# Kernel tuning notes

Hardware: AMD Instinct MI355X
Metric: run time of the kernel (lower is better)

## Reference

```python
import jax, jax.numpy as jnp
import numpy as np

E, TOPK = 8, 2
B, S, D, H = 2, 4096, 1024, 2048


def setup_inputs() -> dict:
    key = jax.random.key(0)
    k1, k2, k3, k4, k5 = jax.random.split(key, 5)
    x = jax.random.normal(k1, (B, S, D), dtype=jnp.float32)
    expert_p = jax.random.uniform(k2, (B * S, TOPK), dtype=jnp.float32)
    expert_idxs = jax.random.randint(k3, (B * S, TOPK), 0, E)
    # experts.weight = stack(cat([w1, w3], dim=1)) -> [E, D, 2H]
    w13 = jax.random.normal(k4, (E, D, 2 * H), dtype=jnp.float32) * 0.02
    # output_experts.weight = stack(w2) -> [E, H, D]
    w2 = jax.random.normal(k5, (E, H, D), dtype=jnp.float32) * 0.02
    return {"x": x, "expert_p": expert_p, "expert_idxs": expert_idxs, "w13": w13, "w2": w2}


def reference(x, expert_p, expert_idxs, w13, w2):
    # Faithful math of FusedExperts.forward:
    #   per routed pair (t, k) with expert e = expert_idxs[t, k]:
    #     hg = x_t @ w13[e];  h, g = split(hg)   (h from w1, g from w3)
    #     y_t += expert_p[t, k] * (silu(g) * h) @ w2[e]
    # Expressed as a small static loop over experts with per-token routing mask
    # (the original's sort/grouped-GEMM/scatter is a kernel-level optimization
    # of exactly this computation).
    x_shape = x.shape
    xf = x.reshape(-1, x_shape[-1])  # [T, D]
    n_experts = w13.shape[0]
    y = jnp.zeros_like(xf)
    for e in range(n_experts):
        hg = xf @ w13[e]                       # [T, 2H]
        h, g = jnp.split(hg, 2, axis=-1)       # w1 out, w3 out
        he = jax.nn.silu(g) * h                # [T, H]
        ye = he @ w2[e]                        # [T, D]
        pe = jnp.sum(expert_p * (expert_idxs == e), axis=-1)  # [T]
        y = y + pe[:, None] * ye
    return y.reshape(x_shape)
```

## Files before the change

### kernel.cpp

```cpp
#include <hip/hip_runtime.h>
#include <cstdint>
#include <cstddef>

#define TT   8192
#define DD   1024
#define HH   2048
#define H2   4096
#define EE   8
#define PP   16384
#define PADROWS 17280
#define MAXTILES 135

typedef unsigned short u16;
typedef __attribute__((ext_vector_type(8))) short bf16x8;
typedef __attribute__((ext_vector_type(8))) unsigned short u16x8;
typedef __attribute__((ext_vector_type(4))) float f32x4;

__device__ __forceinline__ u16 f2bf(float f) {
  unsigned int u = __builtin_bit_cast(unsigned int, f);
  u += 0x7fffu + ((u >> 16) & 1u);
  return (u16)(u >> 16);
}
__device__ __forceinline__ float bf2f(u16 s) {
  unsigned int u = ((unsigned int)s) << 16;
  return __builtin_bit_cast(float, u);
}

__device__ __forceinline__ void gload_lds16(const u16* g, u16* l) {
  __builtin_amdgcn_global_load_lds(
      (const __attribute__((address_space(1))) void*)g,
      (__attribute__((address_space(3))) void*)l, 16, 0, 0);
}

__global__ __launch_bounds__(256)
void prep_kernel(const float* __restrict__ x, u16* __restrict__ xb,
                 const float* __restrict__ w13, u16* __restrict__ w13t,
                 const float* __restrict__ w2, u16* __restrict__ w2t,
                 const int* __restrict__ eidx, const float* __restrict__ ep,
                 int* __restrict__ pofs, int* __restrict__ ptok,
                 float* __restrict__ pscale, int* __restrict__ ppos) {
  __shared__ __align__(16) u16 tile[32][140];
  __shared__ int hcnt[EE], hbase[EE], hrun[EE];
  const int b = blockIdx.x;
  const int t = threadIdx.x;

  if (b < 4096) {
    const long i = (long)b * 256 + t;
    const f32x4* s = (const f32x4*)(x + i * 8);
    f32x4 a = s[0], c = s[1];
    u16x8 o;
    o[0]=f2bf(a[0]); o[1]=f2bf(a[1]); o[2]=f2bf(a[2]); o[3]=f2bf(a[3]);
    o[4]=f2bf(c[0]); o[5]=f2bf(c[1]); o[6]=f2bf(c[2]); o[7]=f2bf(c[3]);
    *(u16x8*)(xb + i * 8) = o;
    return;
  }

  if (b < 16384) {
    const float* src; u16* dst; int R, C, gx, gy, gz;
    if (b < 12288) {
      const int lb = b - 4096;
      src = w13; dst = w13t; R = DD; C = H2;
      gx = lb & 127; gy = (lb >> 7) & 7; gz = lb >> 10;
    } else {
      const int lb = b - 12288;
      src = w2; dst = w2t; R = HH; C = DD;
      gx = lb & 31; gy = (lb >> 5) & 15; gz = lb >> 9;
    }
    const long base = (long)gz * (long)R * C;
    const int c0 = gx * 32, r0 = gy * 128;
    {
      const int tx = t & 31, ty = t >> 5;
#pragma unroll
      for (int rr = 0; rr < 16; ++rr) {
        const int r = ty + rr * 8;
        tile[tx][r] = f2bf(src[base + (long)(r0 + r) * C + c0 + tx]);
      }
    }
    __syncthreads();
    {
      const int k = t & 15, cb = t >> 4;
#pragma unroll
      for (int i = 0; i < 2; ++i) {
        const int c = i * 16 + cb;
        u16x8 o = *(const u16x8*)(&tile[c][8 * k]);
        *(u16x8*)(dst + base + (long)(c0 + c) * R + r0 + 8 * k) = o;
      }
    }
    return;
  }

  if (t < EE) { hcnt[t] = 0; hrun[t] = 0; }
  __syncthreads();
#pragma unroll 4
  for (int k = 0; k < 64; ++k) {
    const int i = t * 64 + k;
    atomicAdd(&hcnt[eidx[i]], 1);
  }
  __syncthreads();
  if (t == 0) {
    int run = 0;
#pragma unroll
    for (int e = 0; e < EE; ++e) {
      pofs[e] = run; hbase[e] = run;
      run += ((hcnt[e] + 127) >> 7) << 7;
    }
    pofs[EE] = run;
  }
  __syncthreads();
#pragma unroll 4
  for (int k = 0; k < 64; ++k) {
    const int i = t * 64 + k;
    const int e = eidx[i];
    const int r = atomicAdd(&hrun[e], 1);
    const int pos = hbase[e] + r;
    ptok[pos] = i >> 1;
    pscale[pos] = ep[i];
    ppos[i] = pos;
  }
}

__global__ __launch_bounds__(256, 2)
void gemm1_kernel(const u16* __restrict__ xb, const u16* __restrict__ w13t,
                  const int* __restrict__ ptok, const int* __restrict__ pofs,
                  u16* __restrict__ hb) {
  __shared__ __align__(16) u16 lds_a[128 * 64];
  __shared__ __align__(16) u16 lds_b[128 * 64];

  const int f = blockIdx.y * MAXTILES + blockIdx.x;
  const int wg = (f & 7) * 540 + (f >> 3);
  const int tileIdx = wg % MAXTILES;
  const int j = wg / MAXTILES;

  const int ts = tileIdx * 128;
  if (ts >= pofs[EE]) return;
  int e = 0;
#pragma unroll
  for (int i = 1; i < EE; ++i) e += (ts >= pofs[i]) ? 1 : 0;

  const int tid = threadIdx.x;
  const int w = tid >> 6, lane = tid & 63;
  const int wr = w >> 1, wc = w & 1;

  const u16* bbase = w13t + (long)e * ((long)H2 * DD);

  const u16* asrc[4]; const u16* bsrc[4];
  u16* adst[4]; u16* bdst[4];
#pragma unroll
  for (int r = 0; r < 4; ++r) {
    const int L = (r * 4 + w) * 1024 + lane * 16;
    const int row = L >> 7;
    const int slot = ((L >> 4) & 7) ^ (row & 7);
    asrc[r] = xb + (long)ptok[ts + row] * DD + slot * 8;
    const int gr = (row < 64) ? (j * 64 + row) : (HH + j * 64 + row - 64);
    bsrc[r] = bbase + (long)gr * DD + slot * 8;
    adst[r] = lds_a + (r * 4 + w) * 512;
    bdst[r] = lds_b + (r * 4 + w) * 512;
  }

  const int rA = wr * 64 + (lane & 15);
  const int sA = lane >> 4;
  const int x7 = lane & 7;
  int aoff[2][4], boff[2][4];
  int rB[4];
  rB[0] = wc * 32 + (lane & 15);
  rB[1] = wc * 32 + 16 + (lane & 15);
  rB[2] = 64 + wc * 32 + (lane & 15);
  rB[3] = 64 + wc * 32 + 16 + (lane & 15);
#pragma unroll
  for (int kk = 0; kk < 2; ++kk) {
    const int sl = ((kk * 4 + sA) ^ x7) * 8;
#pragma unroll
    for (int m = 0; m < 4; ++m) aoff[kk][m] = (rA + m * 16) * 64 + sl;
#pragma unroll
    for (int n = 0; n < 4; ++n) boff[kk][n] = rB[n] * 64 + sl;
  }

  f32x4 acc[4][4];
#pragma unroll
  for (int m = 0; m < 4; ++m)
#pragma unroll
    for (int n = 0; n < 4; ++n) acc[m][n] = (f32x4){0.f, 0.f, 0.f, 0.f};

  for (int k0 = 0; k0 < DD; k0 += 64) {
#pragma unroll
    for (int r = 0; r < 4; ++r) gload_lds16(asrc[r] + k0, adst[r]);
#pragma unroll
    for (int r = 0; r < 4; ++r) gload_lds16(bsrc[r] + k0, bdst[r]);
    __syncthreads();

    bf16x8 af[2][4], bfr[2][4];
#pragma unroll
    for (int kk = 0; kk < 2; ++kk) {
#pragma unroll
      for (int m = 0; m < 4; ++m) af[kk][m] = *(const bf16x8*)(lds_a + aoff[kk][m]);
#pragma unroll
      for (int n = 0; n < 4; ++n) bfr[kk][n] = *(const bf16x8*)(lds_b + boff[kk][n]);
    }
#pragma unroll
    for (int m = 0; m < 4; ++m)
#pragma unroll
      for (int n = 0; n < 4; ++n)
#pragma unroll
        for (int kk = 0; kk < 2; ++kk)
          acc[m][n] = __builtin_amdgcn_mfma_f32_16x16x32_bf16(af[kk][m], bfr[kk][n], acc[m][n], 0, 0, 0);
    __syncthreads();
  }

  const int rg = lane >> 4;
#pragma unroll
  for (int m = 0; m < 4; ++m)
#pragma unroll
    for (int n = 0; n < 2; ++n) {
      const int col = j * 64 + wc * 32 + n * 16 + (lane & 15);
#pragma unroll
      for (int r = 0; r < 4; ++r) {
        const int row = ts + wr * 64 + m * 16 + rg * 4 + r;
        const float h = acc[m][n][r];
        const float g = acc[m][n + 2][r];
        hb[(long)row * HH + col] = f2bf(h * (g / (1.f + __expf(-g))));
      }
    }
}

__global__ __launch_bounds__(256, 2)
void gemm2_kernel(const u16* __restrict__ hb, const u16* __restrict__ w2t,
                  const float* __restrict__ pscale, const int* __restrict__ pofs,
                  u16* __restrict__ ye) {
  __shared__ __align__(16) u16 lds_a[128 * 64];
  __shared__ __align__(16) u16 lds_b[256 * 64];

  const int f = blockIdx.y * 136 + blockIdx.x;
  const int k8 = f & 7, idx = f >> 3;
  const int tileIdx = (k8 & 1) * 68 + idx;
  const int j = k8 >> 1;

  const int ts = tileIdx * 128;
  if (ts >= pofs[EE]) return;
  int e = 0;
#pragma unroll
  for (int i = 1; i < EE; ++i) e += (ts >= pofs[i]) ? 1 : 0;

  const int tid = threadIdx.x;
  const int w = tid >> 6, lane = tid & 63;
  const int wr = w >> 1, wc = w & 1;

  const u16* bbase = w2t + (long)e * ((long)DD * HH);

  const u16* asrc[4]; const u16* bsrc[8];
  u16* adst[4]; u16* bdst[8];
#pragma unroll
  for (int r = 0; r < 4; ++r) {
    const int L = r * 4096 + tid * 16;
    const int row = L >> 7;
    const int slot = ((L >> 4) & 7) ^ (row & 7);
    asrc[r] = hb + (long)(ts + row) * HH + slot * 8;
    adst[r] = lds_a + r * 2048 + w * 512;
  }
#pragma unroll
  for (int r = 0; r < 8; ++r) {
    const int L = r * 4096 + tid * 16;
    const int row = L >> 7;
    const int slot = ((L >> 4) & 7) ^ (row & 7);
    bsrc[r] = bbase + (long)(j * 256 + row) * HH + slot * 8;
    bdst[r] = lds_b + r * 2048 + w * 512;
  }

  const int l15 = lane & 15, x7 = lane & 7, sA = lane >> 4;
  int aoff[2][4], boff[2][8];
#pragma unroll
  for (int kk = 0; kk < 2; ++kk) {
    const int sl = ((kk * 4 + sA) ^ x7) * 8;
#pragma unroll
    for (int m = 0; m < 4; ++m) aoff[kk][m] = (wr * 64 + m * 16 + l15) * 64 + sl;
#pragma unroll
    for (int n = 0; n < 8; ++n) boff[kk][n] = (wc * 128 + n * 16 + l15) * 64 + sl;
  }

  f32x4 acc[4][8];
#pragma unroll
  for (int m = 0; m < 4; ++m)
#pragma unroll
    for (int n = 0; n < 8; ++n) acc[m][n] = (f32x4){0.f, 0.f, 0.f, 0.f};

  for (int k0 = 0; k0 < HH; k0 += 64) {
#pragma unroll
    for (int r = 0; r < 4; ++r) gload_lds16(asrc[r] + k0, adst[r]);
#pragma unroll
    for (int r = 0; r < 8; ++r) gload_lds16(bsrc[r] + k0, bdst[r]);
    __syncthreads();

    bf16x8 af[2][4], bfr[2][8];
#pragma unroll
    for (int kk = 0; kk < 2; ++kk) {
#pragma unroll
      for (int m = 0; m < 4; ++m) af[kk][m] = *(const bf16x8*)(lds_a + aoff[kk][m]);
#pragma unroll
      for (int n = 0; n < 8; ++n) bfr[kk][n] = *(const bf16x8*)(lds_b + boff[kk][n]);
    }
#pragma unroll
    for (int m = 0; m < 4; ++m)
#pragma unroll
      for (int n = 0; n < 8; ++n)
#pragma unroll
        for (int kk = 0; kk < 2; ++kk)
          acc[m][n] = __builtin_amdgcn_mfma_f32_16x16x32_bf16(af[kk][m], bfr[kk][n], acc[m][n], 0, 0, 0);
    __syncthreads();
  }

#pragma unroll
  for (int m = 0; m < 4; ++m)
#pragma unroll
    for (int r = 0; r < 4; ++r) {
      const int row = ts + wr * 64 + m * 16 + sA * 4 + r;
      const float sc = pscale[row];
#pragma unroll
      for (int n = 0; n < 8; ++n) {
        const int col = j * 256 + wc * 128 + n * 16 + l15;
        ye[(long)row * DD + col] = f2bf(acc[m][n][r] * sc);
      }
    }
}

__global__ void combine_kernel(const u16* __restrict__ ye, const int* __restrict__ ppos,
                               float* __restrict__ y) {
  const long i = (long)blockIdx.x * 256 + threadIdx.x;
  const int t = (int)(i >> 7);
  const int c = ((int)i & 127) * 8;
  const int p0 = ppos[t * 2], p1 = ppos[t * 2 + 1];
  u16x8 v0 = *(const u16x8*)(ye + (long)p0 * DD + c);
  u16x8 v1 = *(const u16x8*)(ye + (long)p1 * DD + c);
  f32x4 o0, o1;
  o0[0] = bf2f(v0[0]) + bf2f(v1[0]);
  o0[1] = bf2f(v0[1]) + bf2f(v1[1]);
  o0[2] = bf2f(v0[2]) + bf2f(v1[2]);
  o0[3] = bf2f(v0[3]) + bf2f(v1[3]);
  o1[0] = bf2f(v0[4]) + bf2f(v1[4]);
  o1[1] = bf2f(v0[5]) + bf2f(v1[5]);
  o1[2] = bf2f(v0[6]) + bf2f(v1[6]);
  o1[3] = bf2f(v0[7]) + bf2f(v1[7]);
  *(f32x4*)(y + (long)t * DD + c) = o0;
  *(f32x4*)(y + (long)t * DD + c + 4) = o1;
}

extern "C" void kernel_launch(void* const* d_in, const int* in_sizes, int n_in,
                              void* d_out, int out_size, void* d_ws, size_t ws_size,
                              hipStream_t stream) {
  const float* x    = (const float*)d_in[0];
  const float* ep   = (const float*)d_in[1];
  const int*   eidx = (const int*)d_in[2];
  const float* w13  = (const float*)d_in[3];
  const float* w2   = (const float*)d_in[4];
  float* y = (float*)d_out;

  char* ws = (char*)d_ws;
  size_t off = 0;
  auto alloc = [&](size_t bytes) {
    char* p = ws + off;
    off = (off + bytes + 255) & ~(size_t)255;
    return p;
  };
  u16* xb     = (u16*)alloc((size_t)TT * DD * 2);
  u16* w13t   = (u16*)alloc((size_t)EE * H2 * DD * 2);
  u16* w2t    = (u16*)alloc((size_t)EE * DD * HH * 2);
  u16* hb     = (u16*)alloc((size_t)PADROWS * HH * 2);
  u16* ye     = (u16*)alloc((size_t)PADROWS * DD * 2);
  char* zbase = ws + off;
  int*   ptok   = (int*)alloc((size_t)PADROWS * 4);
  float* pscale = (float*)alloc((size_t)PADROWS * 4);
  size_t zbytes = (size_t)((ws + off) - zbase);
  int*   pofs   = (int*)alloc((EE + 1) * 4);
  int*   ppos   = (int*)alloc((size_t)PP * 4);
  (void)ws_size; (void)in_sizes; (void)n_in; (void)out_size;

  hipMemsetAsync(zbase, 0, zbytes, stream);

  prep_kernel<<<16385, 256, 0, stream>>>(x, xb, w13, w13t, w2, w2t,
                                         eidx, ep, pofs, ptok, pscale, ppos);

  gemm1_kernel<<<dim3(MAXTILES, HH / 64), 256, 0, stream>>>(xb, w13t, ptok, pofs, hb);
  gemm2_kernel<<<dim3(136, 4), 256, 0, stream>>>(hb, w2t, pscale, pofs, ye);
  combine_kernel<<<4096, 256, 0, stream>>>(ye, ppos, y);
}
```

Measured before the change: 358.1 us.

## Rewrite gemm1 as 256x256 tile, 8-wave, double-buffered pipelined MFMA kernel

gemm1 now uses 512 threads and a 256-row by 128-column (h/g interleaved) tile with a 128 KB double-buffered LDS ring. Global-to-LDS loads for the next K-steps are interleaved between quarter blocks of MFMAs, using explicit vmcnt/lgkmcnt waits, barriers and setprio. The goal is to hide load latency and raise arithmetic intensity per tile. Expert groups are padded to 256 rows to match, and gemm2's grid remap is adjusted for the new padding. This adds padding waste and relies on delicate manual synchronization, with only one block able to fit per CU.

```diff
diff --git a/kernel.cpp b/kernel.cpp
--- a/kernel.cpp
+++ b/kernel.cpp
@@ -8,8 +8,8 @@
 #define H2   4096
 #define EE   8
 #define PP   16384
-#define PADROWS 17280
-#define MAXTILES 135
+#define PADROWS 18432
+#define MAXT1 72
 
 typedef unsigned short u16;
 typedef __attribute__((ext_vector_type(8))) short bf16x8;
@@ -31,6 +31,11 @@
       (const __attribute__((address_space(1))) void*)g,
       (__attribute__((address_space(3))) void*)l, 16, 0, 0);
 }
+
+#define BAR()    __builtin_amdgcn_s_barrier()
+#define LGKM0()  asm volatile("s_waitcnt lgkmcnt(0)")
+#define WAITV4() asm volatile("s_waitcnt vmcnt(4)" ::: "memory")
+#define WAITV0() asm volatile("s_waitcnt vmcnt(0)" ::: "memory")
 
 __global__ __launch_bounds__(256)
 void prep_kernel(const float* __restrict__ x, u16* __restrict__ xb,
@@ -102,7 +107,7 @@
 #pragma unroll
     for (int e = 0; e < EE; ++e) {
       pofs[e] = run; hbase[e] = run;
-      run += ((hcnt[e] + 127) >> 7) << 7;
+      run += ((hcnt[e] + 255) >> 8) << 8;
     }
     pofs[EE] = run;
   }
@@ -119,19 +124,28 @@
   }
 }
 
-__global__ __launch_bounds__(256, 2)
+#define QUAD(M0, N0) do {                                                        \
+    __builtin_amdgcn_s_setprio(1);                                               \
+    _Pragma("unroll") for (int mm = 0; mm < 4; ++mm)                             \
+    _Pragma("unroll") for (int nn = 0; nn < 2; ++nn)                             \
+    _Pragma("unroll") for (int kk = 0; kk < 2; ++kk)                             \
+      acc[(M0)+mm][(N0)+nn] = __builtin_amdgcn_mfma_f32_16x16x32_bf16(           \
+          af[kk][(M0)+mm], bf[kk][(N0)+nn], acc[(M0)+mm][(N0)+nn], 0, 0, 0);     \
+    __builtin_amdgcn_s_setprio(0);                                               \
+  } while (0)
+
+__global__ __launch_bounds__(512)
 void gemm1_kernel(const u16* __restrict__ xb, const u16* __restrict__ w13t,
                   const int* __restrict__ ptok, const int* __restrict__ pofs,
                   u16* __restrict__ hb) {
-  __shared__ __align__(16) u16 lds_a[128 * 64];
-  __shared__ __align__(16) u16 lds_b[128 * 64];
-
-  const int f = blockIdx.y * MAXTILES + blockIdx.x;
-  const int wg = (f & 7) * 540 + (f >> 3);
-  const int tileIdx = wg % MAXTILES;
-  const int j = wg / MAXTILES;
-
-  const int ts = tileIdx * 128;
+  __shared__ __align__(16) u16 lds[65536];
+
+  const int f = blockIdx.y * MAXT1 + blockIdx.x;
+  const int wg = (f & 7) * 144 + (f >> 3);
+  const int tileIdx = wg % MAXT1;
+  const int j = wg / MAXT1;
+
+  const int ts = tileIdx * 256;
   if (ts >= pofs[EE]) return;
   int e = 0;
 #pragma unroll
@@ -139,82 +153,109 @@
 
   const int tid = threadIdx.x;
   const int w = tid >> 6, lane = tid & 63;
-  const int wr = w >> 1, wc = w & 1;
+  const int wm = w >> 2, wn = w & 3;
 
   const u16* bbase = w13t + (long)e * ((long)H2 * DD);
 
-  const u16* asrc[4]; const u16* bsrc[4];
-  u16* adst[4]; u16* bdst[4];
-#pragma unroll
-  for (int r = 0; r < 4; ++r) {
-    const int L = (r * 4 + w) * 1024 + lane * 16;
-    const int row = L >> 7;
-    const int slot = ((L >> 4) & 7) ^ (row & 7);
-    asrc[r] = xb + (long)ptok[ts + row] * DD + slot * 8;
-    const int gr = (row < 64) ? (j * 64 + row) : (HH + j * 64 + row - 64);
-    bsrc[r] = bbase + (long)gr * DD + slot * 8;
-    adst[r] = lds_a + (r * 4 + w) * 512;
-    bdst[r] = lds_b + (r * 4 + w) * 512;
-  }
-
-  const int rA = wr * 64 + (lane & 15);
-  const int sA = lane >> 4;
-  const int x7 = lane & 7;
-  int aoff[2][4], boff[2][4];
-  int rB[4];
-  rB[0] = wc * 32 + (lane & 15);
-  rB[1] = wc * 32 + 16 + (lane & 15);
-  rB[2] = 64 + wc * 32 + (lane & 15);
-  rB[3] = 64 + wc * 32 + 16 + (lane & 15);
+  int aoffg[2][2]; int boffg[2][2]; int dstA[2][2], dstB[2][2];
+#pragma unroll
+  for (int ht = 0; ht < 2; ++ht)
+#pragma unroll
+    for (int i = 0; i < 2; ++i) {
+      const int L = tid * 16 + i * 8192;
+      const int row = L >> 7;
+      const int slot = ((L >> 4) & 7) ^ (row & 7);
+      aoffg[ht][i] = ptok[ts + ht * 128 + row] * DD + slot * 8;
+      const int r = ht * 128 + row;
+      const int wnr = r >> 6, within = r & 63;
+      const int grow = (within < 32) ? (j * 128 + wnr * 32 + within)
+                                     : (HH + j * 128 + wnr * 32 + within - 32);
+      boffg[ht][i] = grow * DD + slot * 8;
+      dstA[ht][i] = ht * 8192 + i * 4096 + w * 512;
+      dstB[ht][i] = 32768 + ht * 8192 + i * 4096 + w * 512;
+    }
+
+  const int l15 = lane & 15, x7 = lane & 7, sA = lane >> 4;
+  int aoff[2][8], boff[2][4];
 #pragma unroll
   for (int kk = 0; kk < 2; ++kk) {
     const int sl = ((kk * 4 + sA) ^ x7) * 8;
 #pragma unroll
-    for (int m = 0; m < 4; ++m) aoff[kk][m] = (rA + m * 16) * 64 + sl;
-#pragma unroll
-    for (int n = 0; n < 4; ++n) boff[kk][n] = rB[n] * 64 + sl;
-  }
-
-  f32x4 acc[4][4];
-#pragma unroll
-  for (int m = 0; m < 4; ++m)
+    for (int m = 0; m < 8; ++m) aoff[kk][m] = (m * 16 + l15) * 64 + sl;
+#pragma unroll
+    for (int n = 0; n < 4; ++n) boff[kk][n] = ((w & 1) * 64 + n * 16 + l15) * 64 + sl;
+  }
+
+  f32x4 acc[8][4];
+#pragma unroll
+  for (int m = 0; m < 8; ++m)
 #pragma unroll
     for (int n = 0; n < 4; ++n) acc[m][n] = (f32x4){0.f, 0.f, 0.f, 0.f};
 
-  for (int k0 = 0; k0 < DD; k0 += 64) {
-#pragma unroll
-    for (int r = 0; r < 4; ++r) gload_lds16(asrc[r] + k0, adst[r]);
-#pragma unroll
-    for (int r = 0; r < 4; ++r) gload_lds16(bsrc[r] + k0, bdst[r]);
-    __syncthreads();
-
-    bf16x8 af[2][4], bfr[2][4];
+  auto stageA = [&](int t, int p, int ht) {
+    const int k0 = t * 64;
+    gload_lds16(xb + aoffg[ht][0] + k0, lds + p * 16384 + dstA[ht][0]);
+    gload_lds16(xb + aoffg[ht][1] + k0, lds + p * 16384 + dstA[ht][1]);
+  };
+  auto stageB = [&](int t, int p, int ht) {
+    const int k0 = t * 64;
+    gload_lds16(bbase + boffg[ht][0] + k0, lds + p * 16384 + dstB[ht][0]);
+    gload_lds16(bbase + boffg[ht][1] + k0, lds + p * 16384 + dstB[ht][1]);
+  };
+
+  bf16x8 af[2][8], bf[2][4];
+
+  stageA(0, 0, 0); stageA(0, 0, 1); stageB(0, 0, 0); stageB(0, 0, 1);
+  stageA(1, 1, 0); stageA(1, 1, 1);
+  WAITV4(); BAR();
+
+  for (int t = 0; t < 16; ++t) {
+    const int p = t & 1;
+    const bool stB = t < 15, stA = t < 14;
+    const u16* Areg = lds + p * 16384 + wm * 8192;
+    const u16* Breg = lds + 32768 + p * 16384 + (wn >> 1) * 8192;
 #pragma unroll
     for (int kk = 0; kk < 2; ++kk) {
 #pragma unroll
-      for (int m = 0; m < 4; ++m) af[kk][m] = *(const bf16x8*)(lds_a + aoff[kk][m]);
-#pragma unroll
-      for (int n = 0; n < 4; ++n) bfr[kk][n] = *(const bf16x8*)(lds_b + boff[kk][n]);
-    }
-#pragma unroll
-    for (int m = 0; m < 4; ++m)
-#pragma unroll
-      for (int n = 0; n < 4; ++n)
-#pragma unroll
-        for (int kk = 0; kk < 2; ++kk)
-          acc[m][n] = __builtin_amdgcn_mfma_f32_16x16x32_bf16(af[kk][m], bfr[kk][n], acc[m][n], 0, 0, 0);
-    __syncthreads();
-  }
-
-  const int rg = lane >> 4;
-#pragma unroll
-  for (int m = 0; m < 4; ++m)
+      for (int m = 0; m < 4; ++m) af[kk][m] = *(const bf16x8*)(Areg + aoff[kk][m]);
+#pragma unroll
+      for (int n = 0; n < 2; ++n) bf[kk][n] = *(const bf16x8*)(Breg + boff[kk][n]);
+    }
+    if (stB) stageB(t + 1, p ^ 1, 0);
+    BAR(); LGKM0();
+    QUAD(0, 0);
+    BAR();
+#pragma unroll
+    for (int kk = 0; kk < 2; ++kk)
+#pragma unroll
+      for (int m = 4; m < 8; ++m) af[kk][m] = *(const bf16x8*)(Areg + aoff[kk][m]);
+    if (stB) stageB(t + 1, p ^ 1, 1);
+    BAR(); LGKM0();
+    QUAD(4, 0);
+    BAR();
+#pragma unroll
+    for (int kk = 0; kk < 2; ++kk)
+#pragma unroll
+      for (int n = 2; n < 4; ++n) bf[kk][n] = *(const bf16x8*)(Breg + boff[kk][n]);
+    if (stA) stageA(t + 2, p, 0);
+    BAR(); LGKM0();
+    QUAD(4, 2);
+    BAR();
+    if (stA) stageA(t + 2, p, 1);
+    BAR();
+    QUAD(0, 2);
+    if (t < 14) { WAITV4(); } else if (t == 14) { WAITV0(); }
+    BAR();
+  }
+
+#pragma unroll
+  for (int m = 0; m < 8; ++m)
 #pragma unroll
     for (int n = 0; n < 2; ++n) {
-      const int col = j * 64 + wc * 32 + n * 16 + (lane & 15);
+      const int col = j * 128 + wn * 32 + n * 16 + l15;
 #pragma unroll
       for (int r = 0; r < 4; ++r) {
-        const int row = ts + wr * 64 + m * 16 + rg * 4 + r;
+        const int row = ts + wm * 128 + m * 16 + sA * 4 + r;
         const float h = acc[m][n][r];
         const float g = acc[m][n + 2][r];
         hb[(long)row * HH + col] = f2bf(h * (g / (1.f + __expf(-g))));
@@ -229,9 +270,9 @@
   __shared__ __align__(16) u16 lds_a[128 * 64];
   __shared__ __align__(16) u16 lds_b[256 * 64];
 
-  const int f = blockIdx.y * 136 + blockIdx.x;
+  const int f = blockIdx.y * 72 + blockIdx.x;
   const int k8 = f & 7, idx = f >> 3;
-  const int tileIdx = (k8 & 1) * 68 + idx;
+  const int tileIdx = (k8 & 1) * 72 + idx;
   const int j = k8 >> 1;
 
   const int ts = tileIdx * 128;
@@ -377,7 +418,7 @@
   prep_kernel<<<16385, 256, 0, stream>>>(x, xb, w13, w13t, w2, w2t,
                                          eidx, ep, pofs, ptok, pscale, ppos);
 
-  gemm1_kernel<<<dim3(MAXTILES, HH / 64), 256, 0, stream>>>(xb, w13t, ptok, pofs, hb);
-  gemm2_kernel<<<dim3(136, 4), 256, 0, stream>>>(hb, w2t, pscale, pofs, ye);
+  gemm1_kernel<<<dim3(MAXT1, HH / 128), 512, 0, stream>>>(xb, w13t, ptok, pofs, hb);
+  gemm2_kernel<<<dim3(72, 8), 256, 0, stream>>>(hb, w2t, pscale, pofs, ye);
   combine_kernel<<<4096, 256, 0, stream>>>(ye, ppos, y);
 }
```

Result: no change. 361.2 us (+0.9%).
